# Optimization experiments

Measured on AMD Instinct MI355X. Metric: run time of the kernel, lower is better.

Reference implementation:

```python
import jax, jax.numpy as jnp
import numpy as np

N_HEAD, D_HEAD = 10, 38
D_MODEL, D_INNER = 380, 900
QLEN, BSZ = 1024, 4
MIN_LEN, MAX_LEN = -1024, 1024
EPS = 1e-5
SCALE = 1.0 / D_HEAD ** 0.5


def _ln(x, g, b):
    m = x.mean(-1, keepdims=True)
    v = ((x - m) ** 2).mean(-1, keepdims=True)
    return (x - m) / jnp.sqrt(v + EPS) * g + b


def setup_inputs() -> dict:
    key = jax.random.key(0)
    ks = jax.random.split(key, 10)
    s = 0.02
    w = jax.random.normal(ks[0], (QLEN, BSZ, D_MODEL), jnp.float32)
    # sinusoidal relative position embeddings over positions max_len .. min_len
    pos = jnp.arange(MAX_LEN, MIN_LEN - 1, -1, dtype=jnp.float32)  # [rlen]
    inv_freq = 1.0 / (10000.0 ** (jnp.arange(0, D_MODEL, 2, dtype=jnp.float32) / D_MODEL))
    sin_inp = pos[:, None] * inv_freq[None, :]
    r = jnp.concatenate([jnp.sin(sin_inp), jnp.cos(sin_inp)], axis=-1)  # [rlen, d_model]
    # causal mask, True = attend; layout [qlen, klen, bsz]
    attn_mask = jnp.broadcast_to(jnp.tril(jnp.ones((QLEN, QLEN), bool))[:, :, None], (QLEN, QLEN, BSZ))
    attn_relpos = jax.random.randint(ks[1], (BSZ, QLEN, QLEN), MIN_LEN, MAX_LEN + 1).astype(jnp.int32)
    return {
        'w': w,
        'r': r,
        'r_w_bias': s * jax.random.normal(ks[2], (N_HEAD, D_HEAD), jnp.float32),
        'r_r_bias': s * jax.random.normal(ks[3], (N_HEAD, D_HEAD), jnp.float32),
        'qkv_w': s * jax.random.normal(ks[4], (3 * N_HEAD * D_HEAD, D_MODEL), jnp.float32),
        'r_w': s * jax.random.normal(ks[5], (N_HEAD * D_HEAD, D_MODEL), jnp.float32),
        'o_w': s * jax.random.normal(ks[6], (D_MODEL, N_HEAD * D_HEAD), jnp.float32),
        'ln1_g': jnp.ones(D_MODEL, jnp.float32), 'ln1_b': jnp.zeros(D_MODEL, jnp.float32),
        'ff_w1': s * jax.random.normal(ks[7], (D_INNER, D_MODEL), jnp.float32),
        'ff_b1': jnp.zeros(D_INNER, jnp.float32),
        'ff_w2': s * jax.random.normal(ks[8], (D_MODEL, D_INNER), jnp.float32),
        'ff_b2': jnp.zeros(D_MODEL, jnp.float32),
        'ln2_g': jnp.ones(D_MODEL, jnp.float32), 'ln2_b': jnp.zeros(D_MODEL, jnp.float32),
        'attn_mask': attn_mask,
        'attn_relpos': attn_relpos,
        'min_len': MIN_LEN,
        'max_len': MAX_LEN,
    }


def reference(w, r, r_w_bias, r_r_bias, qkv_w, r_w, o_w, ln1_g, ln1_b,
              ff_w1, ff_b1, ff_w2, ff_b2, ln2_g, ln2_b,
              attn_mask, attn_relpos, min_len, max_len):
    qlen, bsz, _ = w.shape
    # qkv projection (no mems, post-lnorm)
    heads = jnp.einsum('ibm,hm->ibh', w, qkv_w)  # [q, b, 3*nh*dh]
    q, k, v = jnp.split(heads, 3, axis=-1)
    q = q.reshape(qlen, bsz, N_HEAD, D_HEAD)
    k = k.reshape(qlen, bsz, N_HEAD, D_HEAD)
    v = v.reshape(qlen, bsz, N_HEAD, D_HEAD)
    rk = (r @ r_w.T).reshape(-1, N_HEAD, D_HEAD)  # [rlen, nh, dh]
    # content score AC and position score BD (Transformer-XL)
    AC = jnp.einsum('ibnd,jbnd->ijbn', q + r_w_bias, k)   # [q, k, b, n]
    BD = jnp.einsum('ibnd,jnd->ijbn', q + r_r_bias, rk)   # [q, rlen, b, n]
    # gather-based relative position indexing (attn_relpos path)
    idx = (max_len - jnp.clip(attn_relpos, min_len, max_len)).transpose(1, 2, 0)  # [q, k, b]
    idx4 = jnp.broadcast_to(idx[..., None], idx.shape + (N_HEAD,))
    BD = jnp.take_along_axis(BD, idx4, axis=1)            # [q, k, b, n]
    score = (AC + BD) * SCALE
    score = jnp.where(attn_mask[:, :, :, None], score, -jnp.inf)
    prob = jax.nn.softmax(score, axis=1)
    vec = jnp.einsum('ijbn,jbnd->ibnd', prob, v).reshape(qlen, bsz, N_HEAD * D_HEAD)
    attn_out = vec @ o_w.T
    out = _ln(w + attn_out, ln1_g, ln1_b)
    # position-wise FF, post-lnorm
    core = jax.nn.relu(out @ ff_w1.T + ff_b1) @ ff_w2.T + ff_b2
    return _ln(out + core, ln2_g, ln2_b)
```

## Files before the change

kernel.cpp:

```cpp
#include <hip/hip_runtime.h>
#include <math.h>

#define QLEN 1024
#define BSZ 4
#define NH 10
#define DH 38
#define DM 380
#define DI 900
#define H3 1140
#define RLEN 2049
#define RLP 2112
#define SCALE 0.16222142113076254f

typedef unsigned short ushortt;
typedef __attribute__((ext_vector_type(8))) short short8;
typedef __attribute__((ext_vector_type(4))) float float4v;

__device__ __forceinline__ float bf2f(ushortt u) {
    return __uint_as_float(((unsigned int)u) << 16);
}
__device__ __forceinline__ ushortt f2bf(float f) {
    unsigned int u = __float_as_uint(f);
    u += 0x7fffu + ((u >> 16) & 1u);
    return (ushortt)(u >> 16);
}

__device__ __forceinline__ void convseg(const float* src, ushortt* dst,
                                        int R, int C, int Rp, int Cp,
                                        int tid0, int stride) {
    const int total = Rp * Cp;
    for (int i = tid0; i < total; i += stride) {
        int r = i / Cp, c = i - r * Cp;
        float v = (r < R && c < C) ? src[(size_t)r * C + c] : 0.f;
        dst[i] = f2bf(v);
    }
}

__global__ __launch_bounds__(256)
void prep_all(const float* __restrict__ w,    ushortt* __restrict__ w_bf,
              const float* __restrict__ qkv,  ushortt* __restrict__ qkv_bf,
              const float* __restrict__ r,    ushortt* __restrict__ r_bf,
              const float* __restrict__ rw,   ushortt* __restrict__ rw_bf,
              const float* __restrict__ ow,   ushortt* __restrict__ ow_bf,
              const float* __restrict__ f1,   ushortt* __restrict__ f1_bf,
              const float* __restrict__ f2,   ushortt* __restrict__ f2_bf,
              float* __restrict__ qwp, ushortt* __restrict__ Kb, ushortt* __restrict__ Vb,
              ushortt* __restrict__ qr_bf, ushortt* __restrict__ rk_bf,
              ushortt* __restrict__ vec) {
    const int stride = gridDim.x * 256;
    const int tid0 = blockIdx.x * 256 + threadIdx.x;
    convseg(w,   w_bf,   4096, DM, 4096, 384, tid0, stride);
    convseg(qkv, qkv_bf, H3,   DM, 1152, 384, tid0, stride);
    convseg(r,   r_bf,   RLEN, DM, 2176, 384, tid0, stride);
    convseg(rw,  rw_bf,  DM,   DM, 384,  384, tid0, stride);
    convseg(ow,  ow_bf,  DM,   DM, 384,  384, tid0, stride);
    convseg(f1,  f1_bf,  DI,   DM, 960,  384, tid0, stride);
    convseg(f2,  f2_bf,  DM,   DI, 384,  928, tid0, stride);
    for (int i = tid0; i < BSZ * NH * 1024 * 2; i += stride) {
        size_t idx = (size_t)(i >> 1) * 40 + 38 + (i & 1);
        qwp[idx] = 0.f; Kb[idx] = 0; Vb[idx] = 0;
    }
    for (int i = tid0; i < 4096 * 4; i += stride)
        vec[(size_t)(i >> 2) * 384 + 380 + (i & 3)] = 0;
    for (int i = tid0; i < BSZ * NH * 1024 * 26; i += stride) {
        int row = i / 26, c = 38 + i % 26;
        qr_bf[(size_t)row * 64 + c] = 0;
    }
    for (int i = tid0; i < NH * RLP * 26; i += stride) {
        int row = i / 26, c = 38 + i % 26;
        rk_bf[(size_t)row * 64 + c] = 0;
    }
    for (int i = tid0; i < NH * 63 * 64; i += stride) {
        int n = i / (63 * 64), rem = i % (63 * 64);
        rk_bf[((size_t)n * RLP + RLEN + rem / 64) * 64 + rem % 64] = 0;
    }
}

template<int EPI>
__global__ __launch_bounds__(256)
void gemm_mfma(const ushortt* __restrict__ A, const ushortt* __restrict__ B,
               const float* __restrict__ bias, void* __restrict__ Cout,
               int M, int N, int Kpp, int ldc,
               const float* __restrict__ bias2, float* __restrict__ out2,
               float* __restrict__ out3, float* __restrict__ out4) {
    __shared__ __align__(16) ushortt As[128 * 32];
    __shared__ __align__(16) ushortt Bs[64 * 32];
    const int tid = threadIdx.x;
    const int wid = tid >> 6, lane = tid & 63;
    const int bRow = blockIdx.y * 128, bCol = blockIdx.x * 64;

    float4v acc[2][4];
    const float4v zz = {0.f, 0.f, 0.f, 0.f};
    #pragma unroll
    for (int m = 0; m < 2; ++m)
        #pragma unroll
        for (int n = 0; n < 4; ++n) acc[m][n] = zz;

    const int arow = tid >> 1, acol = (tid & 1) * 16;
    const int brow = tid >> 2, bcol = (tid & 3) * 8;
    const int fr = lane & 15, kg = lane >> 4;

    for (int k0 = 0; k0 < Kpp; k0 += 32) {
        const ushortt* ag = A + (size_t)(bRow + arow) * Kpp + k0 + acol;
        float4v a0 = *(const float4v*)ag;
        float4v a1 = *(const float4v*)(ag + 8);
        const ushortt* bg = B + (size_t)(bCol + brow) * Kpp + k0 + bcol;
        float4v b0 = *(const float4v*)bg;
        __syncthreads();
        *(float4v*)&As[arow * 32 + acol] = a0;
        *(float4v*)&As[arow * 32 + acol + 8] = a1;
        *(float4v*)&Bs[brow * 32 + bcol] = b0;
        __syncthreads();

        short8 bf[4];
        #pragma unroll
        for (int n = 0; n < 4; ++n)
            bf[n] = *(const short8*)&Bs[(n * 16 + fr) * 32 + kg * 8];
        #pragma unroll
        for (int m = 0; m < 2; ++m) {
            short8 af = *(const short8*)&As[(wid * 32 + m * 16 + fr) * 32 + kg * 8];
            #pragma unroll
            for (int n = 0; n < 4; ++n)
                acc[m][n] = __builtin_amdgcn_mfma_f32_16x16x32_bf16(af, bf[n], acc[m][n], 0, 0, 0);
        }
    }

    #pragma unroll
    for (int m = 0; m < 2; ++m)
        #pragma unroll
        for (int n = 0; n < 4; ++n)
            #pragma unroll
            for (int j = 0; j < 4; ++j) {
                const int row = bRow + wid * 32 + m * 16 + (lane >> 4) * 4 + j;
                const int col = bCol + n * 16 + (lane & 15);
                const float v = acc[m][n][j];
                if (EPI == 0) {
                    if (row < M && col < N) ((float*)Cout)[(size_t)row * ldc + col] = v;
                } else if (EPI == 3) {
                    if (row < M && col < 928) {
                        float h = (col < DI) ? fmaxf(v + bias[col], 0.f) : 0.f;
                        ((ushortt*)Cout)[(size_t)row * 928 + col] = f2bf(h);
                    }
                } else if (EPI == 4) {
                    if (row < M && col < N) ((float*)Cout)[(size_t)row * ldc + col] = v + bias[col];
                } else if (EPI == 5) {
                    if (col < H3) {
                        int part = col / 380;
                        int c = col - part * 380;
                        int nh = c / 38, d = c - nh * 38;
                        int q = row >> 2, b2 = row & 3;
                        size_t idx = (((size_t)b2 * NH + nh) * 1024 + q) * 40 + d;
                        if (part == 0) {
                            ((float*)Cout)[idx] = v + bias[c];
                            ((ushortt*)out2)[(((size_t)b2 * NH + nh) * 1024 + q) * 64 + d]
                                = f2bf(v + bias2[c]);
                        } else if (part == 1) ((ushortt*)out3)[idx] = f2bf(v);
                        else ((ushortt*)out4)[idx] = f2bf(v);
                    }
                } else {
                    if (row < RLEN && col < DM) {
                        int nh = col / 38, d = col - nh * 38;
                        ((ushortt*)Cout)[((size_t)nh * RLP + row) * 64 + d] = f2bf(v);
                    }
                }
            }
}

__global__ __launch_bounds__(256)
void bd_gemm(const ushortt* __restrict__ qr, const ushortt* __restrict__ rk,
             ushortt* __restrict__ BD, int bofs) {
    __shared__ __align__(16) ushortt As[64][72];
    __shared__ __align__(16) ushortt Bs[32][72];
    __shared__ __align__(16) ushortt Call[64 * 32 * 10];
    const int tid = threadIdx.x;
    const int wid = tid >> 6, lane = tid & 63;
    const int jt = blockIdx.x, qt = blockIdx.y, lb = blockIdx.z;
    const int j0 = jt * 32, q0 = qt * 64;
    const int fr = lane & 15, kg = lane >> 4;
    const int jcount = min(32, RLEN - j0);

    for (int n = 0; n < NH; ++n) {
        const ushortt* Ab = qr + (((size_t)(bofs + lb) * NH + n) * 1024 + q0) * 64;
        const ushortt* Bb = rk + ((size_t)n * RLP + j0) * 64;
        __syncthreads();
        {
            int rr = tid >> 2, cc = (tid & 3) * 16;
            *(float4v*)&As[rr][cc] = *(const float4v*)(Ab + (size_t)rr * 64 + cc);
            *(float4v*)&As[rr][cc + 8] = *(const float4v*)(Ab + (size_t)rr * 64 + cc + 8);
            int br = tid >> 3, bc = (tid & 7) * 8;
            *(float4v*)&Bs[br][bc] = *(const float4v*)(Bb + (size_t)br * 64 + bc);
        }
        __syncthreads();
        float4v acc[2] = {{0.f,0.f,0.f,0.f},{0.f,0.f,0.f,0.f}};
        #pragma unroll
        for (int ks = 0; ks < 64; ks += 32) {
            short8 af = *(const short8*)&As[wid * 16 + fr][ks + kg * 8];
            #pragma unroll
            for (int c = 0; c < 2; ++c) {
                short8 bfr = *(const short8*)&Bs[c * 16 + fr][ks + kg * 8];
                acc[c] = __builtin_amdgcn_mfma_f32_16x16x32_bf16(af, bfr, acc[c], 0, 0, 0);
            }
        }
        #pragma unroll
        for (int c = 0; c < 2; ++c)
            #pragma unroll
            for (int jj = 0; jj < 4; ++jj) {
                int rq = wid * 16 + (lane >> 4) * 4 + jj;
                int cj = c * 16 + (lane & 15);
                Call[(rq * 32 + cj) * 10 + n] = f2bf(acc[c][jj]);
            }
    }
    __syncthreads();
    const int rowdw = jcount * 5;
    const unsigned* Cdw = (const unsigned*)Call;
    unsigned* G = (unsigned*)BD;
    for (int idx = tid; idx < 64 * rowdw; idx += 256) {
        int rr = idx / rowdw, rem = idx - rr * rowdw;
        size_t gdw = ((((size_t)lb * 1024 + q0 + rr) * RLEN + j0) * 10) / 2 + rem;
        G[gdw] = Cdw[rr * 160 + rem];
    }
}

__global__ __launch_bounds__(256)
void attn5(const float* __restrict__ qwp, const ushortt* __restrict__ Kp,
           const ushortt* __restrict__ Vp, const ushortt* __restrict__ BD,
           const int* __restrict__ relpos,
           ushortt* __restrict__ op, float2* __restrict__ ml, int b0, int nb) {
    const int bid = blockIdx.x;
    const int xcd = bid & 7, t = bid >> 3;
    const int gl = t / 10, n = t - gl * 10;
    const int G = gl * 8 + xcd;
    int qc, lb, s;
    {
        const int c3 = 32 * nb, c2 = 24 * nb, c1 = 16 * nb;
        if (G < c3)                { qc = 31 - G / (4 * nb); int r2 = G % (4 * nb); lb = r2 >> 2; s = r2 & 3; }
        else if (G < c3 + c2)      { int l2 = G - c3; qc = 23 - l2 / (3 * nb); int r2 = l2 % (3 * nb); lb = r2 / 3; s = r2 % 3; }
        else if (G < c3 + c2 + c1) { int l2 = G - c3 - c2; qc = 15 - l2 / (2 * nb); int r2 = l2 % (2 * nb); lb = r2 >> 1; s = r2 & 1; }
        else                       { int l2 = G - c3 - c2 - c1; qc = 7 - l2 / nb; lb = l2 % nb; s = 0; }
    }
    const int ns = (qc >> 3) + 1;
    const int qbase = qc * 32;
    const int b = b0 + lb;
    const int tid = threadIdx.x;
    const int row = tid >> 3, kg = tid & 7;
    const int qi = qbase + row;
    const size_t bn = (size_t)b * NH + n;
    const size_t prow = ((size_t)s * (BSZ * NH) + bn) * 1024 + qi;

    const int ntiles = (qbase + 95) >> 6;

    __shared__ __align__(16) float KtL[64 * 40];
    __shared__ __align__(16) float VtL[64 * 40];
    __shared__ float pL[32 * 66];

    const ushortt* Kbase = Kp + bn * 1024 * 40;
    const ushortt* Vbase = Vp + bn * 1024 * 40;

    float4v qw[10];
    {
        const float4v* src = (const float4v*)(qwp + (bn * 1024 + qi) * 40);
        #pragma unroll
        for (int i = 0; i < 10; ++i) qw[i] = src[i];
    }
    float o[5] = {0.f, 0.f, 0.f, 0.f, 0.f};
    float mrun = -INFINITY, lrun = 0.f;
    const int* rp = relpos + ((size_t)b * QLEN + qi) * QLEN;
    const ushortt* bdrow = BD + (((size_t)lb * 1024 + qi) * RLEN) * NH + n;

    for (int kt = s; kt < ntiles; kt += ns) {
        const int k0 = kt * 64;
        __syncthreads();
        {
            const short8* ks = (const short8*)(Kbase + (size_t)k0 * 40);
            const short8* vs = (const short8*)(Vbase + (size_t)k0 * 40);
            for (int e = tid; e < 320; e += 256) {
                short8 kv = ks[e], vv = vs[e];
                float4v k0v, k1v, v0v, v1v;
                #pragma unroll
                for (int x = 0; x < 4; ++x) {
                    k0v[x] = bf2f((ushortt)kv[x]);     k1v[x] = bf2f((ushortt)kv[4 + x]);
                    v0v[x] = bf2f((ushortt)vv[x]);     v1v[x] = bf2f((ushortt)vv[4 + x]);
                }
                ((float4v*)KtL)[e * 2] = k0v; ((float4v*)KtL)[e * 2 + 1] = k1v;
                ((float4v*)VtL)[e * 2] = v0v; ((float4v*)VtL)[e * 2 + 1] = v1v;
            }
        }
        __syncthreads();

        int jv[8];
        #pragma unroll
        for (int ss = 0; ss < 8; ++ss) {
            const int kk = k0 + kg + ss * 8;
            int j = -1;
            if (kk <= qi) {
                int rpv = rp[kk];
                rpv = rpv < -1024 ? -1024 : (rpv > 1024 ? 1024 : rpv);
                j = 1024 - rpv;
            }
            jv[ss] = j;
        }
        float bdv[8];
        #pragma unroll
        for (int ss = 0; ss < 8; ++ss)
            bdv[ss] = (jv[ss] >= 0) ? bf2f(bdrow[(size_t)jv[ss] * NH]) : 0.f;

        float sarr[8];
        float pmax = -INFINITY;
        #pragma unroll
        for (int ss = 0; ss < 8; ++ss) {
            float sv = -INFINITY;
            if (jv[ss] >= 0) {
                const int k = kg + ss * 8;
                float acc1 = 0.f;
                const float4v* kt4 = (const float4v*)(KtL + k * 40);
                #pragma unroll
                for (int i = 0; i < 10; ++i) {
                    float4v kv = kt4[i];
                    acc1 += qw[i][0] * kv[0] + qw[i][1] * kv[1]
                          + qw[i][2] * kv[2] + qw[i][3] * kv[3];
                }
                sv = (acc1 + bdv[ss]) * SCALE;
            }
            sarr[ss] = sv;
            pmax = fmaxf(pmax, sv);
        }
        pmax = fmaxf(pmax, __shfl_xor(pmax, 1, 64));
        pmax = fmaxf(pmax, __shfl_xor(pmax, 2, 64));
        pmax = fmaxf(pmax, __shfl_xor(pmax, 4, 64));
        const float nm = fmaxf(mrun, pmax);
        const float corr = __expf(mrun - nm);
        float psum = 0.f;
        float* prw = pL + row * 66;
        #pragma unroll
        for (int ss = 0; ss < 8; ++ss) {
            float p = __expf(sarr[ss] - nm);
            psum += p;
            prw[kg + ss * 8] = p;
        }
        psum += __shfl_xor(psum, 1, 64);
        psum += __shfl_xor(psum, 2, 64);
        psum += __shfl_xor(psum, 4, 64);
        lrun = lrun * corr + psum;
        mrun = nm;
        #pragma unroll
        for (int jj = 0; jj < 5; ++jj) o[jj] *= corr;
        int kmax = qi - k0 + 1; if (kmax > 64) kmax = 64;
        #pragma unroll 4
        for (int k = 0; k < kmax; ++k) {
            float p = prw[k];
            const float* vr = VtL + k * 40;
            float4v v4 = *(const float4v*)(vr + 4 * kg);
            float v1 = vr[32 + kg];
            o[0] += p * v4[0]; o[1] += p * v4[1];
            o[2] += p * v4[2]; o[3] += p * v4[3];
            o[4] += p * v1;
        }
    }
    ushortt* oprow = op + prow * 40;
    #pragma unroll
    for (int jj = 0; jj < 4; ++jj) oprow[4 * kg + jj] = f2bf(o[jj]);
    oprow[32 + kg] = f2bf(o[4]);
    if (kg == 0) ml[prow] = make_float2(mrun, lrun);
}

__global__ __launch_bounds__(256)
void attn_combine(const ushortt* __restrict__ op, const float2* __restrict__ ml,
                  ushortt* __restrict__ vec) {
    const int idx = blockIdx.x * 256 + threadIdx.x;
    if (idx >= BSZ * NH * 1024 * 38) return;
    const int d = idx % 38;
    const int rh = idx / 38;
    const int q = rh & 1023;
    const int bn = rh >> 10;
    const int b = bn / NH, n = bn - b * NH;
    const int ns = ((q >> 5) >> 3) + 1;
    const size_t stride = (size_t)BSZ * NH * 1024;
    float M = -INFINITY;
    float2 mv[4];
    for (int sp = 0; sp < ns; ++sp) {
        mv[sp] = ml[sp * stride + rh];
        M = fmaxf(M, mv[sp].x);
    }
    float l = 0.f, o = 0.f;
    for (int sp = 0; sp < ns; ++sp) {
        float w = __expf(mv[sp].x - M);
        l += mv[sp].y * w;
        o += bf2f(op[(sp * stride + rh) * 40 + d]) * w;
    }
    vec[((size_t)q * BSZ + b) * 384 + (size_t)n * 38 + d] = f2bf(o / l);
}

template<bool WRITE_BF>
__global__ __launch_bounds__(256)
void ln_kernel(const float* __restrict__ x1, const float* __restrict__ x2,
               const float* __restrict__ g, const float* __restrict__ bb,
               float* __restrict__ outf, ushortt* __restrict__ outbf) {
    const int row = blockIdx.x;
    const float* p1 = x1 + (size_t)row * DM;
    const float* p2 = x2 + (size_t)row * DM;
    __shared__ float xb[DM];
    __shared__ float red[256];
    const int tid = threadIdx.x;
    float s = 0.f;
    for (int i = tid; i < DM; i += 256) { float v = p1[i] + p2[i]; xb[i] = v; s += v; }
    red[tid] = s; __syncthreads();
    for (int st = 128; st > 0; st >>= 1) { if (tid < st) red[tid] += red[tid + st]; __syncthreads(); }
    const float mean = red[0] / DM;
    __syncthreads();
    float s2 = 0.f;
    for (int i = tid; i < DM; i += 256) { float d = xb[i] - mean; s2 += d * d; }
    red[tid] = s2; __syncthreads();
    for (int st = 128; st > 0; st >>= 1) { if (tid < st) red[tid] += red[tid + st]; __syncthreads(); }
    const float rstd = rsqrtf(red[0] / DM + 1e-5f);
    for (int i = tid; i < (WRITE_BF ? 384 : DM); i += 256) {
        float v = 0.f;
        if (i < DM) {
            v = (xb[i] - mean) * rstd * g[i] + bb[i];
            outf[(size_t)row * DM + i] = v;
        }
        if (WRITE_BF) outbf[(size_t)row * 384 + i] = f2bf(i < DM ? v : 0.f);
    }
}

extern "C" void kernel_launch(void* const* d_in, const int* in_sizes, int n_in,
                              void* d_out, int out_size, void* d_ws, size_t ws_size,
                              hipStream_t stream) {
    const float* w     = (const float*)d_in[0];
    const float* r     = (const float*)d_in[1];
    const float* rwb   = (const float*)d_in[2];
    const float* rrb   = (const float*)d_in[3];
    const float* qkv_w = (const float*)d_in[4];
    const float* r_w   = (const float*)d_in[5];
    const float* o_w   = (const float*)d_in[6];
    const float* ln1g  = (const float*)d_in[7];
    const float* ln1b  = (const float*)d_in[8];
    const float* ffw1  = (const float*)d_in[9];
    const float* ffb1  = (const float*)d_in[10];
    const float* ffw2  = (const float*)d_in[11];
    const float* ffb2  = (const float*)d_in[12];
    const float* ln2g  = (const float*)d_in[13];
    const float* ln2b  = (const float*)d_in[14];
    const int*   relpos = (const int*)d_in[16];
    float* out = (float*)d_out;

    char* cur = (char*)d_ws;
    auto alloc = [&](size_t bytes) { char* p = cur; cur += (bytes + 255) & ~(size_t)255; return p; };
    ushortt* w_bf    = (ushortt*)alloc((size_t)4096 * 384 * 2);
    ushortt* qkv_bf  = (ushortt*)alloc((size_t)1152 * 384 * 2);
    ushortt* r_bf    = (ushortt*)alloc((size_t)2176 * 384 * 2);
    ushortt* rw_bf   = (ushortt*)alloc((size_t)384 * 384 * 2);
    ushortt* ow_bf   = (ushortt*)alloc((size_t)384 * 384 * 2);
    ushortt* f1_bf   = (ushortt*)alloc((size_t)960 * 384 * 2);
    ushortt* f2_bf   = (ushortt*)alloc((size_t)384 * 928 * 2);
    float*   qwp     = (float*)alloc((size_t)BSZ * NH * 1024 * 40 * 4);
    ushortt* K_bf    = (ushortt*)alloc((size_t)BSZ * NH * 1024 * 40 * 2);
    ushortt* V_bf    = (ushortt*)alloc((size_t)BSZ * NH * 1024 * 40 * 2);
    ushortt* qr_bf   = (ushortt*)alloc((size_t)BSZ * NH * 1024 * 64 * 2);
    ushortt* rk_bf   = (ushortt*)alloc((size_t)NH * RLP * 64 * 2);
    ushortt* vec_bf  = (ushortt*)alloc((size_t)4096 * 384 * 2);
    ushortt* out1_bf = (ushortt*)alloc((size_t)4096 * 384 * 2);
    ushortt* h1_bf   = (ushortt*)alloc((size_t)4096 * 928 * 2);
    float*   attnf   = (float*)alloc((size_t)4096 * DM * 4);
    float*   out1f   = (float*)alloc((size_t)4096 * DM * 4);
    float*   core    = (float*)alloc((size_t)4096 * DM * 4);

    ushortt* op_part = (ushortt*)attnf;
    float2*  ml_part = (float2*)((char*)attnf + (size_t)4 * BSZ * NH * 1024 * 40 * 2);

    const size_t bd_b_bytes = (size_t)1024 * RLEN * NH * 2;
    ushortt* BD = (ushortt*)alloc(bd_b_bytes * BSZ);
    bool full = ((size_t)(cur - (char*)d_ws) <= ws_size);
    if (!full) { cur = (char*)BD; BD = (ushortt*)alloc(bd_b_bytes); }

    auto cgrid = [](size_t total) { return dim3((unsigned)((total + 255) / 256)); };
    prep_all<<<dim3(2048), 256, 0, stream>>>(w, w_bf, qkv_w, qkv_bf, r, r_bf,
                                             r_w, rw_bf, o_w, ow_bf, ffw1, f1_bf, ffw2, f2_bf,
                                             qwp, K_bf, V_bf, qr_bf, rk_bf, vec_bf);

    gemm_mfma<5><<<dim3(18, 32), 256, 0, stream>>>(w_bf, qkv_bf, rwb, qwp, 4096, H3, 384, 0,
                                                   rrb, (float*)qr_bf, (float*)K_bf, (float*)V_bf);
    gemm_mfma<6><<<dim3(6, 17), 256, 0, stream>>>(r_bf, rw_bf, nullptr, rk_bf, RLEN, DM, 384, 0,
                                                  nullptr, nullptr, nullptr, nullptr);
    if (full) {
        bd_gemm<<<dim3(65, 16, BSZ), 256, 0, stream>>>(qr_bf, rk_bf, BD, 0);
        attn5<<<dim3(3200), 256, 0, stream>>>(qwp, K_bf, V_bf, BD, relpos,
                                              op_part, ml_part, 0, BSZ);
    } else {
        for (int b = 0; b < BSZ; ++b) {
            bd_gemm<<<dim3(65, 16, 1), 256, 0, stream>>>(qr_bf, rk_bf, BD, b);
            attn5<<<dim3(800), 256, 0, stream>>>(qwp, K_bf, V_bf, BD, relpos,
                                                 op_part, ml_part, b, 1);
        }
    }
    attn_combine<<<cgrid((size_t)BSZ * NH * 1024 * 38), 256, 0, stream>>>(op_part, ml_part, vec_bf);
    gemm_mfma<0><<<dim3(6, 32), 256, 0, stream>>>(vec_bf, ow_bf, nullptr, attnf, 4096, DM, 384, DM,
                                                  nullptr, nullptr, nullptr, nullptr);
    ln_kernel<true><<<4096, 256, 0, stream>>>(w, attnf, ln1g, ln1b, out1f, out1_bf);
    gemm_mfma<3><<<dim3(15, 32), 256, 0, stream>>>(out1_bf, f1_bf, ffb1, h1_bf, 4096, DI, 384, 928,
                                                   nullptr, nullptr, nullptr, nullptr);
    gemm_mfma<4><<<dim3(6, 32), 256, 0, stream>>>(h1_bf, f2_bf, ffb2, core, 4096, DM, 928, DM,
                                                  nullptr, nullptr, nullptr, nullptr);
    ln_kernel<false><<<4096, 256, 0, stream>>>(out1f, core, ln2g, ln2b, out, nullptr);
}
```

Before: 387.3 us.

## Compute attention content scores with bf16 MFMA and remap bd_gemm blocks per XCD

The attention kernel now computes the q·k content scores with bf16 16x16x32 MFMA instructions on tiles in shared memory instead of scalar fp32 dot products. To feed it, q+r_w_bias is stored as padded bf16 (stride 64) rather than fp32, and probabilities are kept as bf16 in a shared buffer that also holds the scores. Separately, bd_gemm moves to a 1D grid whose block index is remapped so that blocks sharing the same q tile land on the same XCD for cache locality. This trades some precision (bf16 scores and probabilities) and an extra barrier per tile for much cheaper score computation.

```diff
diff --git a/kernel.cpp b/kernel.cpp
--- a/kernel.cpp
+++ b/kernel.cpp
@@ -44,7 +44,7 @@
               const float* __restrict__ ow,   ushortt* __restrict__ ow_bf,
               const float* __restrict__ f1,   ushortt* __restrict__ f1_bf,
               const float* __restrict__ f2,   ushortt* __restrict__ f2_bf,
-              float* __restrict__ qwp, ushortt* __restrict__ Kb, ushortt* __restrict__ Vb,
+              ushortt* __restrict__ qw_bf, ushortt* __restrict__ Kb, ushortt* __restrict__ Vb,
               ushortt* __restrict__ qr_bf, ushortt* __restrict__ rk_bf,
               ushortt* __restrict__ vec) {
     const int stride = gridDim.x * 256;
@@ -58,13 +58,14 @@
     convseg(f2,  f2_bf,  DM,   DI, 384,  928, tid0, stride);
     for (int i = tid0; i < BSZ * NH * 1024 * 2; i += stride) {
         size_t idx = (size_t)(i >> 1) * 40 + 38 + (i & 1);
-        qwp[idx] = 0.f; Kb[idx] = 0; Vb[idx] = 0;
+        Kb[idx] = 0; Vb[idx] = 0;
     }
     for (int i = tid0; i < 4096 * 4; i += stride)
         vec[(size_t)(i >> 2) * 384 + 380 + (i & 3)] = 0;
     for (int i = tid0; i < BSZ * NH * 1024 * 26; i += stride) {
         int row = i / 26, c = 38 + i % 26;
         qr_bf[(size_t)row * 64 + c] = 0;
+        qw_bf[(size_t)row * 64 + c] = 0;
     }
     for (int i = tid0; i < NH * RLP * 26; i += stride) {
         int row = i / 26, c = 38 + i % 26;
@@ -149,13 +150,13 @@
                         int c = col - part * 380;
                         int nh = c / 38, d = c - nh * 38;
                         int q = row >> 2, b2 = row & 3;
-                        size_t idx = (((size_t)b2 * NH + nh) * 1024 + q) * 40 + d;
+                        size_t i40 = (((size_t)b2 * NH + nh) * 1024 + q) * 40 + d;
+                        size_t i64 = (((size_t)b2 * NH + nh) * 1024 + q) * 64 + d;
                         if (part == 0) {
-                            ((float*)Cout)[idx] = v + bias[c];
-                            ((ushortt*)out2)[(((size_t)b2 * NH + nh) * 1024 + q) * 64 + d]
-                                = f2bf(v + bias2[c]);
-                        } else if (part == 1) ((ushortt*)out3)[idx] = f2bf(v);
-                        else ((ushortt*)out4)[idx] = f2bf(v);
+                            ((ushortt*)Cout)[i64] = f2bf(v + bias[c]);
+                            ((ushortt*)out2)[i64] = f2bf(v + bias2[c]);
+                        } else if (part == 1) ((ushortt*)out3)[i40] = f2bf(v);
+                        else ((ushortt*)out4)[i40] = f2bf(v);
                     }
                 } else {
                     if (row < RLEN && col < DM) {
@@ -168,13 +169,17 @@
 
 __global__ __launch_bounds__(256)
 void bd_gemm(const ushortt* __restrict__ qr, const ushortt* __restrict__ rk,
-             ushortt* __restrict__ BD, int bofs) {
+             ushortt* __restrict__ BD, int bofs, int nb) {
     __shared__ __align__(16) ushortt As[64][72];
     __shared__ __align__(16) ushortt Bs[32][72];
     __shared__ __align__(16) ushortt Call[64 * 32 * 10];
+    const int bid = blockIdx.x;
+    const int xcd = bid & 7, t = bid >> 3;
+    const int gl = t / 65, jt = t - gl * 65;
+    const int G = gl * 8 + xcd;
+    const int lb = G >> 4, qt = G & 15;
     const int tid = threadIdx.x;
     const int wid = tid >> 6, lane = tid & 63;
-    const int jt = blockIdx.x, qt = blockIdx.y, lb = blockIdx.z;
     const int j0 = jt * 32, q0 = qt * 64;
     const int fr = lane & 15, kg = lane >> 4;
     const int jcount = min(32, RLEN - j0);
@@ -213,16 +218,16 @@
     __syncthreads();
     const int rowdw = jcount * 5;
     const unsigned* Cdw = (const unsigned*)Call;
-    unsigned* G = (unsigned*)BD;
+    unsigned* G2 = (unsigned*)BD;
     for (int idx = tid; idx < 64 * rowdw; idx += 256) {
         int rr = idx / rowdw, rem = idx - rr * rowdw;
         size_t gdw = ((((size_t)lb * 1024 + q0 + rr) * RLEN + j0) * 10) / 2 + rem;
-        G[gdw] = Cdw[rr * 160 + rem];
+        G2[gdw] = Cdw[rr * 160 + rem];
     }
 }
 
 __global__ __launch_bounds__(256)
-void attn5(const float* __restrict__ qwp, const ushortt* __restrict__ Kp,
+void attn6(const ushortt* __restrict__ qwb, const ushortt* __restrict__ Kp,
            const ushortt* __restrict__ Vp, const ushortt* __restrict__ BD,
            const int* __restrict__ relpos,
            ushortt* __restrict__ op, float2* __restrict__ ml, int b0, int nb) {
@@ -242,25 +247,30 @@
     const int qbase = qc * 32;
     const int b = b0 + lb;
     const int tid = threadIdx.x;
+    const int wid = tid >> 6, lane = tid & 63;
     const int row = tid >> 3, kg = tid & 7;
     const int qi = qbase + row;
     const size_t bn = (size_t)b * NH + n;
     const size_t prow = ((size_t)s * (BSZ * NH) + bn) * 1024 + qi;
-
     const int ntiles = (qbase + 95) >> 6;
 
-    __shared__ __align__(16) float KtL[64 * 40];
-    __shared__ __align__(16) float VtL[64 * 40];
-    __shared__ float pL[32 * 66];
+    __shared__ __align__(16) ushortt KtL[64 * 72];
+    __shared__ __align__(16) float   VtL[64 * 40];
+    __shared__ __align__(16) ushortt qwL[32 * 72];
+    __shared__ __align__(16) ushortt sL[32 * 66];
 
     const ushortt* Kbase = Kp + bn * 1024 * 40;
     const ushortt* Vbase = Vp + bn * 1024 * 40;
-
-    float4v qw[10];
+    const int fr = lane & 15;
+    const int kg8 = (lane >> 4) * 8;
+
     {
-        const float4v* src = (const float4v*)(qwp + (bn * 1024 + qi) * 40);
-        #pragma unroll
-        for (int i = 0; i < 10; ++i) qw[i] = src[i];
+        int r = tid >> 3, c = (tid & 7) * 8;
+        *(short8*)&qwL[r * 72 + c] = *(const short8*)(qwb + (bn * 1024 + qbase + r) * 64 + c);
+        for (int i = tid; i < 64 * 24; i += 256) {
+            int rr = i / 24, cc = 40 + i % 24;
+            KtL[rr * 72 + cc] = 0;
+        }
     }
     float o[5] = {0.f, 0.f, 0.f, 0.f, 0.f};
     float mrun = -INFINITY, lrun = 0.f;
@@ -270,18 +280,19 @@
     for (int kt = s; kt < ntiles; kt += ns) {
         const int k0 = kt * 64;
         __syncthreads();
+        for (int e = tid; e < 320; e += 256) {
+            int rr = e / 5, cc = (e % 5) * 8;
+            *(short8*)&KtL[rr * 72 + cc] = *(const short8*)(Kbase + (size_t)(k0 + rr) * 40 + cc);
+        }
         {
-            const short8* ks = (const short8*)(Kbase + (size_t)k0 * 40);
             const short8* vs = (const short8*)(Vbase + (size_t)k0 * 40);
             for (int e = tid; e < 320; e += 256) {
-                short8 kv = ks[e], vv = vs[e];
-                float4v k0v, k1v, v0v, v1v;
+                short8 vv = vs[e];
+                float4v v0v, v1v;
                 #pragma unroll
                 for (int x = 0; x < 4; ++x) {
-                    k0v[x] = bf2f((ushortt)kv[x]);     k1v[x] = bf2f((ushortt)kv[4 + x]);
-                    v0v[x] = bf2f((ushortt)vv[x]);     v1v[x] = bf2f((ushortt)vv[4 + x]);
+                    v0v[x] = bf2f((ushortt)vv[x]); v1v[x] = bf2f((ushortt)vv[4 + x]);
                 }
-                ((float4v*)KtL)[e * 2] = k0v; ((float4v*)KtL)[e * 2 + 1] = k1v;
                 ((float4v*)VtL)[e * 2] = v0v; ((float4v*)VtL)[e * 2 + 1] = v1v;
             }
         }
@@ -304,23 +315,32 @@
         for (int ss = 0; ss < 8; ++ss)
             bdv[ss] = (jv[ss] >= 0) ? bf2f(bdrow[(size_t)jv[ss] * NH]) : 0.f;
 
+        {
+            const int mt = wid >> 1, ctb = (wid & 1) * 2;
+            short8 a0 = *(const short8*)&qwL[(mt * 16 + fr) * 72 + kg8];
+            short8 a1 = *(const short8*)&qwL[(mt * 16 + fr) * 72 + 32 + kg8];
+            #pragma unroll
+            for (int c = 0; c < 2; ++c) {
+                const int ct = ctb + c;
+                short8 b0f = *(const short8*)&KtL[(ct * 16 + fr) * 72 + kg8];
+                short8 b1f = *(const short8*)&KtL[(ct * 16 + fr) * 72 + 32 + kg8];
+                float4v acc = {0.f, 0.f, 0.f, 0.f};
+                acc = __builtin_amdgcn_mfma_f32_16x16x32_bf16(a0, b0f, acc, 0, 0, 0);
+                acc = __builtin_amdgcn_mfma_f32_16x16x32_bf16(a1, b1f, acc, 0, 0, 0);
+                #pragma unroll
+                for (int j = 0; j < 4; ++j)
+                    sL[(mt * 16 + (lane >> 4) * 4 + j) * 66 + ct * 16 + fr] = f2bf(acc[j]);
+            }
+        }
+        __syncthreads();
+
         float sarr[8];
         float pmax = -INFINITY;
         #pragma unroll
         for (int ss = 0; ss < 8; ++ss) {
             float sv = -INFINITY;
-            if (jv[ss] >= 0) {
-                const int k = kg + ss * 8;
-                float acc1 = 0.f;
-                const float4v* kt4 = (const float4v*)(KtL + k * 40);
-                #pragma unroll
-                for (int i = 0; i < 10; ++i) {
-                    float4v kv = kt4[i];
-                    acc1 += qw[i][0] * kv[0] + qw[i][1] * kv[1]
-                          + qw[i][2] * kv[2] + qw[i][3] * kv[3];
-                }
-                sv = (acc1 + bdv[ss]) * SCALE;
-            }
+            if (jv[ss] >= 0)
+                sv = (bf2f(sL[row * 66 + kg + ss * 8]) + bdv[ss]) * SCALE;
             sarr[ss] = sv;
             pmax = fmaxf(pmax, sv);
         }
@@ -330,12 +350,12 @@
         const float nm = fmaxf(mrun, pmax);
         const float corr = __expf(mrun - nm);
         float psum = 0.f;
-        float* prw = pL + row * 66;
+        ushortt* prw = sL + row * 66;
         #pragma unroll
         for (int ss = 0; ss < 8; ++ss) {
             float p = __expf(sarr[ss] - nm);
             psum += p;
-            prw[kg + ss * 8] = p;
+            prw[kg + ss * 8] = f2bf(p);
         }
         psum += __shfl_xor(psum, 1, 64);
         psum += __shfl_xor(psum, 2, 64);
@@ -347,7 +367,7 @@
         int kmax = qi - k0 + 1; if (kmax > 64) kmax = 64;
         #pragma unroll 4
         for (int k = 0; k < kmax; ++k) {
-            float p = prw[k];
+            float p = bf2f(prw[k]);
             const float* vr = VtL + k * 40;
             float4v v4 = *(const float4v*)(vr + 4 * kg);
             float v1 = vr[32 + kg];
@@ -452,7 +472,7 @@
     ushortt* ow_bf   = (ushortt*)alloc((size_t)384 * 384 * 2);
     ushortt* f1_bf   = (ushortt*)alloc((size_t)960 * 384 * 2);
     ushortt* f2_bf   = (ushortt*)alloc((size_t)384 * 928 * 2);
-    float*   qwp     = (float*)alloc((size_t)BSZ * NH * 1024 * 40 * 4);
+    ushortt* qw_bf   = (ushortt*)alloc((size_t)BSZ * NH * 1024 * 64 * 2);
     ushortt* K_bf    = (ushortt*)alloc((size_t)BSZ * NH * 1024 * 40 * 2);
     ushortt* V_bf    = (ushortt*)alloc((size_t)BSZ * NH * 1024 * 40 * 2);
     ushortt* qr_bf   = (ushortt*)alloc((size_t)BSZ * NH * 1024 * 64 * 2);
@@ -475,20 +495,20 @@
     auto cgrid = [](size_t total) { return dim3((unsigned)((total + 255) / 256)); };
     prep_all<<<dim3(2048), 256, 0, stream>>>(w, w_bf, qkv_w, qkv_bf, r, r_bf,
                                              r_w, rw_bf, o_w, ow_bf, ffw1, f1_bf, ffw2, f2_bf,
-                                             qwp, K_bf, V_bf, qr_bf, rk_bf, vec_bf);
-
-    gemm_mfma<5><<<dim3(18, 32), 256, 0, stream>>>(w_bf, qkv_bf, rwb, qwp, 4096, H3, 384, 0,
+                                             qw_bf, K_bf, V_bf, qr_bf, rk_bf, vec_bf);
+
+    gemm_mfma<5><<<dim3(18, 32), 256, 0, stream>>>(w_bf, qkv_bf, rwb, qw_bf, 4096, H3, 384, 0,
                                                    rrb, (float*)qr_bf, (float*)K_bf, (float*)V_bf);
     gemm_mfma<6><<<dim3(6, 17), 256, 0, stream>>>(r_bf, rw_bf, nullptr, rk_bf, RLEN, DM, 384, 0,
                                                   nullptr, nullptr, nullptr, nullptr);
     if (full) {
-        bd_gemm<<<dim3(65, 16, BSZ), 256, 0, stream>>>(qr_bf, rk_bf, BD, 0);
-        attn5<<<dim3(3200), 256, 0, stream>>>(qwp, K_bf, V_bf, BD, relpos,
+        bd_gemm<<<dim3(65 * 16 * BSZ), 256, 0, stream>>>(qr_bf, rk_bf, BD, 0, BSZ);
+        attn6<<<dim3(3200), 256, 0, stream>>>(qw_bf, K_bf, V_bf, BD, relpos,
                                               op_part, ml_part, 0, BSZ);
     } else {
         for (int b = 0; b < BSZ; ++b) {
-            bd_gemm<<<dim3(65, 16, 1), 256, 0, stream>>>(qr_bf, rk_bf, BD, b);
-            attn5<<<dim3(800), 256, 0, stream>>>(qwp, K_bf, V_bf, BD, relpos,
+            bd_gemm<<<dim3(65 * 16), 256, 0, stream>>>(qr_bf, rk_bf, BD, b, 1);
+            attn6<<<dim3(800), 256, 0, stream>>>(qw_bf, K_bf, V_bf, BD, relpos,
                                                  op_part, ml_part, b, 1);
         }
     }
```

Result: faster. 378.7 us (-2.2%).
